# Performance work log

Hardware: AMD Instinct MI355X
Metric: run time of the kernel (lower is better)

The kernel has to match this reference:

```python
import jax, jax.numpy as jnp
import numpy as np

VTH = 0.5      # SNNParameters.vth_init
TAU = 0.25     # SNNParameters.tau_mem
_GAUSS_C = 1.0 / np.sqrt(0.3 * np.pi)  # surrogate-grad scale (unused in fwd)


def _heaviside(v):
    return (v > 0).astype(v.dtype)


def setup_inputs() -> dict:
    key = jax.random.key(0)
    x = jax.random.normal(key, (16, 128, 512, 32), dtype=jnp.float32)
    return {"x": x}


def reference(x):
    # x: [..., T]; LIF recurrence over the last (time) axis.
    xT = jnp.moveaxis(x, -1, 0)  # [T, ...]
    u0 = jnp.zeros(x.shape[:-1], dtype=x.dtype)
    o0 = jnp.zeros(x.shape[:-1], dtype=x.dtype)

    def step(carry, x_t):
        u, o_prev = carry
        u = TAU * u * (1.0 - o_prev) + x_t          # leaky integrate w/ reset
        o = _heaviside(u - VTH)                     # fire
        return (u, o), o

    _, outT = jax.lax.scan(step, (u0, o0), xT)
    return jnp.moveaxis(outT, 0, -1)  # back to [..., T]
```

## Files before the change

kernel.cpp:

```cpp
#include <hip/hip_runtime.h>


constexpr int T = 32;
constexpr float TAU = 0.25f;
constexpr float VTH = 0.5f;
constexpr int QPR = T / 4;
constexpr int WAVE_F4 = 64 * QPR;
constexpr int BLOCK = 256;
constexpr int TILE_F4 = (BLOCK / 64) * WAVE_F4;

__device__ __forceinline__ int swz(int s) { return s ^ ((s >> 3) & 7); }

__global__ __launch_bounds__(256) void LIFSpike_kernel(
    const float* __restrict__ x, float* __restrict__ out) {
    __shared__ float4 tile[TILE_F4];

    const int t = threadIdx.x;
    const int lane = t & 63;
    const int wid = t >> 6;
    const int wbase = wid * WAVE_F4;
    const size_t base = (size_t)blockIdx.x * TILE_F4;

    const float4* __restrict__ xp = reinterpret_cast<const float4*>(x);
    float4* __restrict__ op = reinterpret_cast<float4*>(out);

#pragma unroll
    for (int k = 0; k < QPR; ++k) {
        const int p = wbase + k * 64;
        const int src = swz(p + lane);
        __builtin_amdgcn_global_load_lds(
            (const __attribute__((address_space(1))) void*)(xp + base + src),
            (__attribute__((address_space(3))) void*)(tile + p),
            16, 0, 0);
    }
    asm volatile("s_waitcnt vmcnt(0)" ::: "memory");

    float u = 0.0f, o = 0.0f;
#pragma unroll
    for (int j = 0; j < QPR; ++j) {
        const int phys = t * QPR + (j ^ (t & 7));
        float4 v = tile[phys];
        float4 r;

        u = TAU * u * (1.0f - o) + v.x;
        o = (u > VTH) ? 1.0f : 0.0f;
        r.x = o;

        u = TAU * u * (1.0f - o) + v.y;
        o = (u > VTH) ? 1.0f : 0.0f;
        r.y = o;

        u = TAU * u * (1.0f - o) + v.z;
        o = (u > VTH) ? 1.0f : 0.0f;
        r.z = o;

        u = TAU * u * (1.0f - o) + v.w;
        o = (u > VTH) ? 1.0f : 0.0f;
        r.w = o;

        tile[phys] = r;
    }
    asm volatile("s_waitcnt lgkmcnt(0)" ::: "memory");

#pragma unroll
    for (int k = 0; k < QPR; ++k) {
        const int p = wbase + k * 64 + lane;
        op[base + p] = tile[swz(p)];
    }
}

extern "C" void kernel_launch(void* const* d_in, const int* in_sizes, int n_in,
                              void* d_out, int out_size, void* d_ws, size_t ws_size,
                              hipStream_t stream) {
    const float* x = (const float*)d_in[0];
    float* out = (float*)d_out;
    int total_f4 = in_sizes[0] / 4;
    int grid = total_f4 / TILE_F4;
    LIFSpike_kernel<<<grid, BLOCK, 0, stream>>>(x, out);
}
```

Baseline: 230.8 us.

## Double-buffer LDS tiles per wave and loop over multiple tiles per block

Each block now processes eight tiles instead of one, double-buffering per-wave LDS slices so the global-to-LDS loads for the next tile overlap compute and stores of the current one, with vmcnt waits counted explicitly. Output stores switch to nontemporal stores. This amortises launch and block startup and is meant to hide load latency, but it shrinks the grid eightfold, which lowers the parallelism available for a memory-bound streaming kernel. The hand-counted vmcnt values must account for the outstanding stores, so a miscount could break correctness.

```diff
diff --git a/kernel.cpp b/kernel.cpp
--- a/kernel.cpp
+++ b/kernel.cpp
@@ -7,65 +7,87 @@
 constexpr int QPR = T / 4;
 constexpr int WAVE_F4 = 64 * QPR;
 constexpr int BLOCK = 256;
-constexpr int TILE_F4 = (BLOCK / 64) * WAVE_F4;
+constexpr int WAVES = BLOCK / 64;
+constexpr int TILE_F4 = WAVES * WAVE_F4;
+constexpr int TPB = 8;
+
+typedef float f32x4 __attribute__((ext_vector_type(4)));
 
 __device__ __forceinline__ int swz(int s) { return s ^ ((s >> 3) & 7); }
 
-__global__ __launch_bounds__(256) void LIFSpike_kernel(
+__global__ __launch_bounds__(BLOCK) void LIFSpike_kernel(
     const float* __restrict__ x, float* __restrict__ out) {
-    __shared__ float4 tile[TILE_F4];
+    __shared__ f32x4 buf[WAVES][2][WAVE_F4];
 
     const int t = threadIdx.x;
     const int lane = t & 63;
     const int wid = t >> 6;
-    const int wbase = wid * WAVE_F4;
-    const size_t base = (size_t)blockIdx.x * TILE_F4;
 
-    const float4* __restrict__ xp = reinterpret_cast<const float4*>(x);
-    float4* __restrict__ op = reinterpret_cast<float4*>(out);
+    const f32x4* __restrict__ xp = reinterpret_cast<const f32x4*>(x);
+    f32x4* __restrict__ op = reinterpret_cast<f32x4*>(out);
+
+    const size_t block_base = (size_t)blockIdx.x * TPB * TILE_F4;
+
+    auto issue_loads = [&](int j, int pb) {
+        const size_t tb = block_base + (size_t)j * TILE_F4 + wid * WAVE_F4;
+#pragma unroll
+        for (int k = 0; k < QPR; ++k) {
+            const int p = k * 64;
+            const int src = swz(p + lane);
+            __builtin_amdgcn_global_load_lds(
+                (const __attribute__((address_space(1))) void*)(xp + tb + src),
+                (__attribute__((address_space(3))) void*)(&buf[wid][pb][p]),
+                16, 0, 0);
+        }
+    };
+
+    issue_loads(0, 0);
 
 #pragma unroll
-    for (int k = 0; k < QPR; ++k) {
-        const int p = wbase + k * 64;
-        const int src = swz(p + lane);
-        __builtin_amdgcn_global_load_lds(
-            (const __attribute__((address_space(1))) void*)(xp + base + src),
-            (__attribute__((address_space(3))) void*)(tile + p),
-            16, 0, 0);
-    }
-    asm volatile("s_waitcnt vmcnt(0)" ::: "memory");
+    for (int j = 0; j < TPB; ++j) {
+        const int pb = j & 1;
+        if (j + 1 < TPB) issue_loads(j + 1, pb ^ 1);
 
-    float u = 0.0f, o = 0.0f;
+        if (j == 0 || j == TPB - 1)
+            asm volatile("s_waitcnt vmcnt(8)" ::: "memory");
+        else
+            asm volatile("s_waitcnt vmcnt(16)" ::: "memory");
+
+        f32x4* cur = &buf[wid][pb][0];
+
+        float u = 0.0f, o = 0.0f;
 #pragma unroll
-    for (int j = 0; j < QPR; ++j) {
-        const int phys = t * QPR + (j ^ (t & 7));
-        float4 v = tile[phys];
-        float4 r;
+        for (int jj = 0; jj < QPR; ++jj) {
+            const int phys = lane * QPR + (jj ^ (lane & 7));
+            f32x4 v = cur[phys];
+            f32x4 r;
 
-        u = TAU * u * (1.0f - o) + v.x;
-        o = (u > VTH) ? 1.0f : 0.0f;
-        r.x = o;
+            u = TAU * u * (1.0f - o) + v.x;
+            o = (u > VTH) ? 1.0f : 0.0f;
+            r.x = o;
 
-        u = TAU * u * (1.0f - o) + v.y;
-        o = (u > VTH) ? 1.0f : 0.0f;
-        r.y = o;
+            u = TAU * u * (1.0f - o) + v.y;
+            o = (u > VTH) ? 1.0f : 0.0f;
+            r.y = o;
 
-        u = TAU * u * (1.0f - o) + v.z;
-        o = (u > VTH) ? 1.0f : 0.0f;
-        r.z = o;
+            u = TAU * u * (1.0f - o) + v.z;
+            o = (u > VTH) ? 1.0f : 0.0f;
+            r.z = o;
 
-        u = TAU * u * (1.0f - o) + v.w;
-        o = (u > VTH) ? 1.0f : 0.0f;
-        r.w = o;
+            u = TAU * u * (1.0f - o) + v.w;
+            o = (u > VTH) ? 1.0f : 0.0f;
+            r.w = o;
 
-        tile[phys] = r;
-    }
-    asm volatile("s_waitcnt lgkmcnt(0)" ::: "memory");
+            cur[phys] = r;
+        }
+        asm volatile("s_waitcnt lgkmcnt(0)" ::: "memory");
 
+        const size_t tb = block_base + (size_t)j * TILE_F4 + wid * WAVE_F4;
 #pragma unroll
-    for (int k = 0; k < QPR; ++k) {
-        const int p = wbase + k * 64 + lane;
-        op[base + p] = tile[swz(p)];
+        for (int k = 0; k < QPR; ++k) {
+            const int s = k * 64 + lane;
+            __builtin_nontemporal_store(cur[swz(s)], op + tb + s);
+        }
     }
 }
 
@@ -75,6 +97,7 @@
     const float* x = (const float*)d_in[0];
     float* out = (float*)d_out;
     int total_f4 = in_sizes[0] / 4;
-    int grid = total_f4 / TILE_F4;
+    int n_tiles = total_f4 / TILE_F4;
+    int grid = n_tiles / TPB;
     LIFSpike_kernel<<<grid, BLOCK, 0, stream>>>(x, out);
 }
```

Measured after the change: 233.4 us. No clear change (+1.1%).
